# Kernel optimization log

Hardware: AMD Instinct MI355X
Metric: run time of the kernel (lower is better)

## Reference

```python
import jax, jax.numpy as jnp
import numpy as np

D_MODEL = 1024
N_HEADS = 16
N_KV_HEADS = 4
D_K = D_MODEL // N_HEADS
Q_SIZE = D_MODEL
KV_SIZE = N_KV_HEADS * D_K
QKV_SIZE = Q_SIZE + 2 * KV_SIZE
EPS = 1.1920929e-07  # torch.nn.RMSNorm default eps (fp32 machine eps)
ROPE_BASE = 10000.0


def rms_norm(x, w):
    # normalize over last dim, learned scale (torch nn.RMSNorm)
    return x * jax.lax.rsqrt(jnp.mean(x * x, axis=-1, keepdims=True) + EPS) * w


def rope(x):
    # torchtune RotaryPositionalEmbeddings: interleaved pairs, x is [B,T,H,D]
    T, d = x.shape[1], x.shape[-1]
    inv_freq = 1.0 / (ROPE_BASE ** (jnp.arange(0, d, 2, dtype=jnp.float32) / d))
    ang = jnp.arange(T, dtype=jnp.float32)[:, None] * inv_freq[None, :]  # [T, d/2]
    cos = jnp.cos(ang)[None, :, None, :]
    sin = jnp.sin(ang)[None, :, None, :]
    xr = x.reshape(x.shape[:-1] + (d // 2, 2))
    x1, x2 = xr[..., 0], xr[..., 1]
    out = jnp.stack([x1 * cos - x2 * sin, x1 * sin + x2 * cos], axis=-1)
    return out.reshape(x.shape)


def setup_inputs() -> dict:
    key = jax.random.key(0)
    k1, k2 = jax.random.split(key)
    x = jax.random.normal(k1, (2, 2048, D_MODEL), dtype=jnp.float32)
    qkvo = jax.random.normal(k2, (QKV_SIZE + D_MODEL, D_MODEL), dtype=jnp.float32) * 0.02
    q_norm_w = jnp.ones((D_K,), dtype=jnp.float32)
    k_norm_w = jnp.ones((D_K,), dtype=jnp.float32)
    return {"x": x, "qkvo": qkvo, "q_norm_w": q_norm_w, "k_norm_w": k_norm_w}


def reference(x, qkvo, q_norm_w, k_norm_w):
    B, T, _ = x.shape
    groups = N_HEADS // N_KV_HEADS
    qkv = x @ qkvo[:QKV_SIZE].T  # [B,T,qkv_size]
    Q = qkv[..., :Q_SIZE].reshape(B, T, N_HEADS, D_K)
    K = qkv[..., Q_SIZE:Q_SIZE + KV_SIZE].reshape(B, T, N_KV_HEADS, D_K)
    V = qkv[..., Q_SIZE + KV_SIZE:].reshape(B, T, N_KV_HEADS, D_K)
    Q = rope(rms_norm(Q, q_norm_w))
    K = rope(rms_norm(K, k_norm_w))
    K = jnp.repeat(K, groups, axis=2)  # GQA expand to [B,T,H,D]
    V = jnp.repeat(V, groups, axis=2)
    scale = 1.0 / np.sqrt(D_K).astype(np.float32)
    scores = jnp.einsum('bqhd,bkhd->bhqk', Q, K) * scale
    causal = jnp.tril(jnp.ones((T, T), dtype=bool))
    scores = jnp.where(causal[None, None], scores, jnp.float32(-jnp.inf))
    attn = jax.nn.softmax(scores, axis=-1)
    out = jnp.einsum('bhqk,bkhd->bqhd', attn, V).reshape(B, T, D_MODEL)
    return out @ qkvo[QKV_SIZE:].T
```

## Files before the change

kernel.cpp:

```cpp
#include <hip/hip_runtime.h>
#include <hip/hip_bf16.h>
#include <cstdint>
#include <cstddef>

typedef __bf16 bf16x8 __attribute__((ext_vector_type(8)));
typedef float f32x4 __attribute__((ext_vector_type(4)));

__device__ __forceinline__ unsigned short f2bf(float f) {
    unsigned u = __builtin_bit_cast(unsigned, f);
    u += 0x7FFFu + ((u >> 16) & 1u);
    return (unsigned short)(u >> 16);
}
__device__ __forceinline__ unsigned pk2(float a, float b) {
    typedef __bf16 bf16x2 __attribute__((ext_vector_type(2)));
    bf16x2 h;
    h[0] = (__bf16)a;
    h[1] = (__bf16)b;
    unsigned r;
    __builtin_memcpy(&r, &h, 4);
    return r;
}
__device__ __forceinline__ float fexp2(float x) {
#if __has_builtin(__builtin_amdgcn_exp2f)
    return __builtin_amdgcn_exp2f(x);
#else
    return __expf(x * 0.6931471805599453f);
#endif
}
__device__ __forceinline__ void gld16(const void* g, void* l) {
    __builtin_amdgcn_global_load_lds((const __attribute__((address_space(1))) void*)g,
                                     (__attribute__((address_space(3))) void*)l, 16, 0, 0);
}

__global__ __launch_bounds__(256) void cast_kernel(const float4* __restrict__ x,
                                                   const float4* __restrict__ w,
                                                   ushort4* __restrict__ xbf,
                                                   ushort4* __restrict__ wbf) {
    int i = blockIdx.x * 256 + threadIdx.x;
    const int NX4 = 4096 * 1024 / 4;
    const int NW4 = 2560 * 1024 / 4;
    float4 v;
    ushort4* o;
    if (i < NX4) { v = x[i]; o = xbf + i; }
    else {
        int j = i - NX4;
        if (j >= NW4) return;
        v = w[j]; o = wbf + j;
    }
    ushort4 r;
    r.x = f2bf(v.x); r.y = f2bf(v.y); r.z = f2bf(v.z); r.w = f2bf(v.w);
    *o = r;
}

__global__ __launch_bounds__(256) void gemm_bf16(const ushort* __restrict__ A,
                                                 const ushort* __restrict__ B,
                                                 float* __restrict__ C,
                                                 int M, int N, int K) {
    __shared__ __align__(16) ushort LA[2][4096];
    __shared__ __align__(16) ushort LB[2][8192];
    int tid = threadIdx.x;
    int w = tid >> 6, lane = tid & 63;
    int qm = lane & 15, quad = lane >> 4;

    int nbx = gridDim.x, nby = gridDim.y;
    int nwg = nbx * nby;
    int f = blockIdx.y * nbx + blockIdx.x;
    int q = nwg >> 3, r = nwg & 7;
    int xcd = f & 7, idx = f >> 3;
    int s = (xcd < r ? xcd * (q + 1) : r * (q + 1) + (xcd - r) * q) + idx;
    int m0 = (s / nby) * 64;
    int n0 = (s % nby) * 128;

    int mw = (w & 1) * 32, nw = (w >> 1) * 64;
    int sw = qm & 7;

    f32x4 acc[2][4];
#pragma unroll
    for (int i = 0; i < 2; i++)
#pragma unroll
        for (int j = 0; j < 4; j++) acc[i][j] = (f32x4){0.f, 0.f, 0.f, 0.f};

    int sa[2], ra[2], ga[2];
#pragma unroll
    for (int u = 0; u < 2; u++) {
        sa[u] = tid + u * 256;
        ra[u] = sa[u] >> 3;
        ga[u] = (sa[u] & 7) ^ (ra[u] & 7);
    }
    int sb[4], rb[4], gb[4];
#pragma unroll
    for (int u = 0; u < 4; u++) {
        sb[u] = tid + u * 256;
        rb[u] = sb[u] >> 3;
        gb[u] = (sb[u] & 7) ^ (rb[u] & 7);
    }

    auto do_stage = [&](int k0, int buf) {
#pragma unroll
        for (int u = 0; u < 2; u++)
            gld16(A + (size_t)(m0 + ra[u]) * K + k0 + ga[u] * 8, &LA[buf][sa[u] * 8]);
#pragma unroll
        for (int u = 0; u < 4; u++)
            gld16(B + (size_t)(n0 + rb[u]) * K + k0 + gb[u] * 8, &LB[buf][sb[u] * 8]);
    };

    do_stage(0, 0);
    int buf = 0;
    for (int k0 = 0; k0 < K; k0 += 64, buf ^= 1) {
        __syncthreads();
        if (k0 + 64 < K) do_stage(k0 + 64, buf ^ 1);
        bf16x8 a[2][2], bb[4][2];
#pragma unroll
        for (int mi = 0; mi < 2; mi++)
#pragma unroll
            for (int h = 0; h < 2; h++)
                a[mi][h] = *(const bf16x8*)&LA[buf][((mw + mi * 16 + qm) * 8 + ((h * 4 + quad) ^ sw)) * 8];
#pragma unroll
        for (int ni = 0; ni < 4; ni++)
#pragma unroll
            for (int h = 0; h < 2; h++)
                bb[ni][h] = *(const bf16x8*)&LB[buf][((nw + ni * 16 + qm) * 8 + ((h * 4 + quad) ^ sw)) * 8];
#pragma unroll
        for (int h = 0; h < 2; h++)
#pragma unroll
            for (int mi = 0; mi < 2; mi++)
#pragma unroll
                for (int ni = 0; ni < 4; ni++)
                    acc[mi][ni] = __builtin_amdgcn_mfma_f32_16x16x32_bf16(a[mi][h], bb[ni][h], acc[mi][ni], 0, 0, 0);
    }
#pragma unroll
    for (int mi = 0; mi < 2; mi++)
#pragma unroll
        for (int ni = 0; ni < 4; ni++) {
            int row = m0 + mw + mi * 16 + quad * 4;
            int col = n0 + nw + ni * 16 + qm;
            float* cp = C + (size_t)row * N + col;
#pragma unroll
            for (int r2 = 0; r2 < 4; r2++) cp[(size_t)r2 * N] = acc[mi][ni][r2];
        }
}

__global__ __launch_bounds__(256) void normrope_kernel(const float* __restrict__ qkv,
                                                       const float* __restrict__ qw,
                                                       const float* __restrict__ kw,
                                                       ushort* __restrict__ Q,
                                                       ushort* __restrict__ Kb) {
    int r = blockIdx.x;
    int b = r >> 11;
    int t = r & 2047;
    int tid = threadIdx.x;
    int w = tid >> 6;
    int lane = tid & 63;

    float inv_freq = __expf(-((float)(lane & 62) * (1.0f / 64.0f)) * 9.210340371976184f);
    float sn, cs;
    sincosf((float)t * inv_freq, &sn, &cs);

#pragma unroll
    for (int hg = 0; hg < 5; hg++) {
        int col = hg * 256 + w * 64 + lane;
        float v = qkv[(size_t)r * 1536 + col];
        float ss = v * v;
#pragma unroll
        for (int m = 1; m < 64; m <<= 1) ss += __shfl_xor(ss, m);
        float rinv = rsqrtf(ss * (1.0f / 64.0f) + 1.1920929e-7f);
        float wt = (hg < 4) ? qw[lane] : kw[lane];
        float vn = v * rinv * wt;
        float pr = __shfl_xor(vn, 1);
        float out = (lane & 1) ? fmaf(pr, sn, vn * cs) : fmaf(vn, cs, -pr * sn);
        if (hg < 4) {
            int h = hg * 4 + w;
            Q[((size_t)(b * 16 + h) * 2048 + t) * 64 + lane] = f2bf(out * 0.125f);
        } else {
            Kb[((size_t)(b * 4 + w) * 2048 + t) * 64 + lane] = f2bf(out);
        }
    }
}

__global__ __launch_bounds__(256) void vtrans_kernel(const float* __restrict__ qkv,
                                                     ushort* __restrict__ VT) {
    __shared__ float tile[64][65];
    int bkv = blockIdx.x;
    int t0 = blockIdx.y * 64;
    int b = bkv >> 2;
    int kvh = bkv & 3;
    int tid = threadIdx.x;
    int c = tid & 63;
    int rr = tid >> 6;
#pragma unroll
    for (int p = 0; p < 16; p++) {
        int tl = p * 4 + rr;
        tile[tl][c] = qkv[((size_t)(b * 2048) + t0 + tl) * 1536 + 1280 + kvh * 64 + c];
    }
    __syncthreads();
    int w5 = c & 31;
    int pc = (c & 32) + ((w5 >> 2) & 3) * 8 + (w5 >> 4) * 4 + (w5 & 3);
#pragma unroll
    for (int p = 0; p < 16; p++) {
        int dd = p * 4 + rr;
        VT[((size_t)bkv * 64 + dd) * 2048 + t0 + pc] = f2bf(tile[c][dd]);
    }
}

__global__ __launch_bounds__(256) void attn7_kernel(const ushort* __restrict__ Q,
                                                    const ushort* __restrict__ K,
                                                    const ushort* __restrict__ VT,
                                                    ushort* __restrict__ O) {
    __shared__ __align__(16) ushort KT[2][4096];
    __shared__ __align__(16) ushort VL[2][4096];

    const float LOG2E = 1.4426950408889634f;
    const float C8 = 11.541560327111707f;

    int blk = blockIdx.x;
    int qp = 31 - (blk >> 5);
    int bh = blk & 31;
    int tid = threadIdx.x;
    int w = tid >> 6, lane = tid & 63;
    int qm = lane & 15, quad = lane >> 4;
    int b = bh >> 4, h = bh & 15;
    int bkv = b * 4 + (h >> 2);

    const ushort* Qbh = Q + (size_t)bh * 2048 * 64;
    const ushort* Kbh = K + (size_t)bkv * 2048 * 64;
    const ushort* Vbh = VT + (size_t)bkv * 64 * 2048;
    int sw = qm & 7;

    int s0 = tid, s1 = tid + 256;
    int r0 = s0 >> 3, g0 = (s0 & 7) ^ (r0 & 7);
    int r1 = s1 >> 3, g1 = (s1 & 7) ^ (r1 & 7);

    auto do_stage = [&](int j0, int buf) {
        gld16(Kbh + (size_t)(j0 + r0) * 64 + g0 * 8, &KT[buf][s0 * 8]);
        gld16(Kbh + (size_t)(j0 + r1) * 64 + g1 * 8, &KT[buf][s1 * 8]);
        gld16(Vbh + (size_t)r0 * 2048 + j0 + g0 * 8, &VL[buf][s0 * 8]);
        gld16(Vbh + (size_t)r1 * 2048 + j0 + g1 * 8, &VL[buf][s1 * 8]);
    };

    int nch = qp + 1;
    int q0 = qp * 64 + w * 16;
    const ushort* qptr = Qbh + (size_t)(q0 + qm) * 64 + quad * 8;
    bf16x8 qb0 = *(const bf16x8*)qptr;
    bf16x8 qb1 = *(const bf16x8*)(qptr + 32);
    f32x4 oacc[4];
    float lacc = 0.f;
#pragma unroll
    for (int i = 0; i < 4; i++) oacc[i] = (f32x4){0.f, 0.f, 0.f, 0.f};

    do_stage(0, 0);
    int buf = 0;
#pragma unroll 1
    for (int i = 0; i < nch; i++, buf ^= 1) {
        int j0 = i * 64;
        __syncthreads();
        if (i + 1 < nch) do_stage(j0 + 64, buf ^ 1);

        f32x4 st[4];
#pragma unroll
        for (int tj = 0; tj < 4; tj++) st[tj] = (f32x4){0.f, 0.f, 0.f, 0.f};
#pragma unroll
        for (int tj = 0; tj < 4; tj++) {
            bf16x8 kf0 = *(const bf16x8*)&KT[buf][((16 * tj + qm) * 8 + (quad ^ sw)) * 8];
            bf16x8 kf1 = *(const bf16x8*)&KT[buf][((16 * tj + qm) * 8 + ((4 + quad) ^ sw)) * 8];
            st[tj] = __builtin_amdgcn_mfma_f32_16x16x32_bf16(kf0, qb0, st[tj], 0, 0, 0);
            st[tj] = __builtin_amdgcn_mfma_f32_16x16x32_bf16(kf1, qb1, st[tj], 0, 0, 0);
        }
        if (i == nch - 1) {
#pragma unroll
            for (int tj = 0; tj < 4; tj++)
#pragma unroll
                for (int r = 0; r < 4; r++) {
                    int key = j0 + tj * 16 + quad * 4 + r;
                    if (key > q0 + qm) st[tj][r] = -1e30f;
                }
        }
        float rs = 0.f;
#pragma unroll
        for (int tj = 0; tj < 4; tj++)
#pragma unroll
            for (int r = 0; r < 4; r++) {
                float pv = fexp2(fmaf(st[tj][r], LOG2E, -C8));
                st[tj][r] = pv;
                rs += pv;
            }
        lacc += rs;

        unsigned up[4];
        up[0] = pk2(st[0][0], st[0][1]);
        up[1] = pk2(st[0][2], st[0][3]);
        up[2] = pk2(st[1][0], st[1][1]);
        up[3] = pk2(st[1][2], st[1][3]);
        bf16x8 pf0;
        __builtin_memcpy(&pf0, up, 16);
        up[0] = pk2(st[2][0], st[2][1]);
        up[1] = pk2(st[2][2], st[2][3]);
        up[2] = pk2(st[3][0], st[3][1]);
        up[3] = pk2(st[3][2], st[3][3]);
        bf16x8 pf1;
        __builtin_memcpy(&pf1, up, 16);

#pragma unroll
        for (int dt = 0; dt < 4; dt++) {
            bf16x8 vf0 = *(const bf16x8*)&VL[buf][((16 * dt + qm) * 8 + (quad ^ sw)) * 8];
            bf16x8 vf1 = *(const bf16x8*)&VL[buf][((16 * dt + qm) * 8 + ((4 + quad) ^ sw)) * 8];
            oacc[dt] = __builtin_amdgcn_mfma_f32_16x16x32_bf16(vf0, pf0, oacc[dt], 0, 0, 0);
            oacc[dt] = __builtin_amdgcn_mfma_f32_16x16x32_bf16(vf1, pf1, oacc[dt], 0, 0, 0);
        }
    }
    float l = lacc;
    l += __shfl_xor(l, 16);
    l += __shfl_xor(l, 32);
    float rinv = 1.0f / l;
    uint2 val;
#pragma unroll
    for (int dt = 0; dt < 4; dt++) {
        val.x = pk2(oacc[dt][0] * rinv, oacc[dt][1] * rinv);
        val.y = pk2(oacc[dt][2] * rinv, oacc[dt][3] * rinv);
        *(uint2*)&O[((size_t)(b * 2048) + q0 + qm) * 1024 + h * 64 + dt * 16 + quad * 4] = val;
    }
}

extern "C" void kernel_launch(void* const* d_in, const int* in_sizes, int n_in,
                              void* d_out, int out_size, void* d_ws, size_t ws_size,
                              hipStream_t stream) {
    (void)in_sizes; (void)n_in; (void)out_size; (void)ws_size;
    const float* x    = (const float*)d_in[0];
    const float* qkvo = (const float*)d_in[1];
    const float* qw   = (const float*)d_in[2];
    const float* kw   = (const float*)d_in[3];
    float* out = (float*)d_out;

    char* ws = (char*)d_ws;
    ushort* xbf = (ushort*)(ws + 0);
    ushort* wbf = (ushort*)(ws + 8388608);
    float*  qkv = (float*)(ws + 13631488);
    ushort* Qb  = (ushort*)(ws + 38797312);
    ushort* Kb  = (ushort*)(ws + 47185920);
    ushort* VT  = (ushort*)(ws + 49283072);
    ushort* Ob  = (ushort*)(ws + 51380224);

    cast_kernel<<<6656, 256, 0, stream>>>((const float4*)x, (const float4*)qkvo,
                                          (ushort4*)xbf, (ushort4*)wbf);
    gemm_bf16<<<dim3(64, 12), 256, 0, stream>>>(xbf, wbf, qkv, 4096, 1536, 1024);
    normrope_kernel<<<4096, 256, 0, stream>>>(qkv, qw, kw, Qb, Kb);
    vtrans_kernel<<<dim3(8, 32), 256, 0, stream>>>(qkv, VT);
    attn7_kernel<<<1024, 256, 0, stream>>>(Qb, Kb, VT, Ob);
    gemm_bf16<<<dim3(64, 8), 256, 0, stream>>>(Ob, wbf + (size_t)1536 * 1024, out, 4096, 1024, 1024);
}
```

Before: 157.2 us.

## Fuse RMSNorm, RoPE and V transpose into the QKV GEMM epilogue

The QKV projection GEMM now applies per-head RMSNorm, RoPE and the Q scaling directly in registers, and writes bf16 Q/K in head-major layout. V tiles go through LDS and are written transposed and permuted for the attention kernel. This removes the fp32 qkv intermediate round trip and two separate kernel launches. The cast kernel also precomputes a cos/sin table for RoPE. In exchange the GEMM epilogue does more shuffles and scattered table reads and has a data-dependent branch per tile.

```diff
diff --git a/kernel.cpp b/kernel.cpp
--- a/kernel.cpp
+++ b/kernel.cpp
@@ -35,21 +35,175 @@
 __global__ __launch_bounds__(256) void cast_kernel(const float4* __restrict__ x,
                                                    const float4* __restrict__ w,
                                                    ushort4* __restrict__ xbf,
-                                                   ushort4* __restrict__ wbf) {
+                                                   ushort4* __restrict__ wbf,
+                                                   float2* __restrict__ tab) {
     int i = blockIdx.x * 256 + threadIdx.x;
     const int NX4 = 4096 * 1024 / 4;
     const int NW4 = 2560 * 1024 / 4;
-    float4 v;
-    ushort4* o;
-    if (i < NX4) { v = x[i]; o = xbf + i; }
-    else {
-        int j = i - NX4;
-        if (j >= NW4) return;
-        v = w[j]; o = wbf + j;
-    }
-    ushort4 r;
-    r.x = f2bf(v.x); r.y = f2bf(v.y); r.z = f2bf(v.z); r.w = f2bf(v.w);
-    *o = r;
+    if (i < NX4 + NW4) {
+        float4 v;
+        ushort4* o;
+        if (i < NX4) { v = x[i]; o = xbf + i; }
+        else { v = w[i - NX4]; o = wbf + (i - NX4); }
+        ushort4 r;
+        r.x = f2bf(v.x); r.y = f2bf(v.y); r.z = f2bf(v.z); r.w = f2bf(v.w);
+        *o = r;
+    } else {
+        int k = i - NX4 - NW4;
+        if (k >= 2048 * 32) return;
+        int t = k >> 5, fp = k & 31;
+        float inv = __expf(-(float)(2 * fp) * (1.0f / 64.0f) * 9.210340371976184f);
+        float sn, cs;
+        sincosf((float)t * inv, &sn, &cs);
+        tab[k] = make_float2(cs, sn);
+    }
+}
+
+__global__ __launch_bounds__(256) void gemm_qkv_fused(const ushort* __restrict__ A,
+                                                      const ushort* __restrict__ B,
+                                                      const float2* __restrict__ tab,
+                                                      const float* __restrict__ qw,
+                                                      const float* __restrict__ kw,
+                                                      ushort* __restrict__ Qo,
+                                                      ushort* __restrict__ Ko,
+                                                      ushort* __restrict__ VT) {
+    const int K = 1024;
+    __shared__ __align__(16) ushort LA[2][4096];
+    __shared__ __align__(16) ushort LB[2][8192];
+    int tid = threadIdx.x;
+    int w = tid >> 6, lane = tid & 63;
+    int qm = lane & 15, quad = lane >> 4;
+
+    int nbx = gridDim.x, nby = gridDim.y;
+    int nwg = nbx * nby;
+    int f = blockIdx.y * nbx + blockIdx.x;
+    int q = nwg >> 3, r = nwg & 7;
+    int xcd = f & 7, idx = f >> 3;
+    int s = (xcd < r ? xcd * (q + 1) : r * (q + 1) + (xcd - r) * q) + idx;
+    int m0 = (s / nby) * 64;
+    int n0 = (s % nby) * 128;
+
+    int mw = (w & 1) * 32, nw = (w >> 1) * 64;
+    int sw = qm & 7;
+
+    f32x4 acc[2][4];
+#pragma unroll
+    for (int i = 0; i < 2; i++)
+#pragma unroll
+        for (int j = 0; j < 4; j++) acc[i][j] = (f32x4){0.f, 0.f, 0.f, 0.f};
+
+    int sa[2], ra[2], ga[2];
+#pragma unroll
+    for (int u = 0; u < 2; u++) {
+        sa[u] = tid + u * 256;
+        ra[u] = sa[u] >> 3;
+        ga[u] = (sa[u] & 7) ^ (ra[u] & 7);
+    }
+    int sb[4], rb[4], gb[4];
+#pragma unroll
+    for (int u = 0; u < 4; u++) {
+        sb[u] = tid + u * 256;
+        rb[u] = sb[u] >> 3;
+        gb[u] = (sb[u] & 7) ^ (rb[u] & 7);
+    }
+
+    auto do_stage = [&](int k0, int buf) {
+#pragma unroll
+        for (int u = 0; u < 2; u++)
+            gld16(A + (size_t)(m0 + ra[u]) * K + k0 + ga[u] * 8, &LA[buf][sa[u] * 8]);
+#pragma unroll
+        for (int u = 0; u < 4; u++)
+            gld16(B + (size_t)(n0 + rb[u]) * K + k0 + gb[u] * 8, &LB[buf][sb[u] * 8]);
+    };
+
+    do_stage(0, 0);
+    int buf = 0;
+    for (int k0 = 0; k0 < K; k0 += 64, buf ^= 1) {
+        __syncthreads();
+        if (k0 + 64 < K) do_stage(k0 + 64, buf ^ 1);
+        bf16x8 a[2][2], bb[4][2];
+#pragma unroll
+        for (int mi = 0; mi < 2; mi++)
+#pragma unroll
+            for (int h = 0; h < 2; h++)
+                a[mi][h] = *(const bf16x8*)&LA[buf][((mw + mi * 16 + qm) * 8 + ((h * 4 + quad) ^ sw)) * 8];
+#pragma unroll
+        for (int ni = 0; ni < 4; ni++)
+#pragma unroll
+            for (int h = 0; h < 2; h++)
+                bb[ni][h] = *(const bf16x8*)&LB[buf][((nw + ni * 16 + qm) * 8 + ((h * 4 + quad) ^ sw)) * 8];
+#pragma unroll
+        for (int h = 0; h < 2; h++)
+#pragma unroll
+            for (int mi = 0; mi < 2; mi++)
+#pragma unroll
+                for (int ni = 0; ni < 4; ni++)
+                    acc[mi][ni] = __builtin_amdgcn_mfma_f32_16x16x32_bf16(a[mi][h], bb[ni][h], acc[mi][ni], 0, 0, 0);
+    }
+
+    int head_col0 = n0 + nw;
+    int rowbase = m0 + mw;
+    int b = rowbase >> 11;
+    int t0g = rowbase & 2047;
+    bool isV = (head_col0 >= 1280);
+
+    __syncthreads();
+    if (isV) {
+        ushort* lv = &LA[0][0] + w * 2048;
+#pragma unroll
+        for (int mi = 0; mi < 2; mi++)
+#pragma unroll
+            for (int r2 = 0; r2 < 4; r2++) {
+                int tt = mi * 16 + quad * 4 + r2;
+                int pcl = ((tt >> 2) & 3) * 8 + ((tt >> 4) & 1) * 4 + (tt & 3);
+#pragma unroll
+                for (int ni = 0; ni < 4; ni++)
+                    lv[(ni * 16 + qm) * 32 + pcl] = f2bf(acc[mi][ni][r2]);
+            }
+    } else {
+        bool isQ = (head_col0 < 1024);
+        const float* wp = isQ ? qw : kw;
+        float wt[4];
+#pragma unroll
+        for (int ni = 0; ni < 4; ni++) wt[ni] = wp[ni * 16 + qm];
+        float qs = isQ ? 0.125f : 1.0f;
+        ushort* op = isQ ? (Qo + (size_t)(b * 16 + (head_col0 >> 6)) * 2048 * 64)
+                         : (Ko + (size_t)(b * 4 + ((head_col0 - 1024) >> 6)) * 2048 * 64);
+#pragma unroll
+        for (int mi = 0; mi < 2; mi++)
+#pragma unroll
+            for (int r2 = 0; r2 < 4; r2++) {
+                float ssum = acc[mi][0][r2] * acc[mi][0][r2] + acc[mi][1][r2] * acc[mi][1][r2]
+                           + acc[mi][2][r2] * acc[mi][2][r2] + acc[mi][3][r2] * acc[mi][3][r2];
+                ssum += __shfl_xor(ssum, 1);
+                ssum += __shfl_xor(ssum, 2);
+                ssum += __shfl_xor(ssum, 4);
+                ssum += __shfl_xor(ssum, 8);
+                float rinv = rsqrtf(ssum * (1.0f / 64.0f) + 1.1920929e-7f);
+                int t = t0g + mi * 16 + quad * 4 + r2;
+#pragma unroll
+                for (int ni = 0; ni < 4; ni++) {
+                    float vn = acc[mi][ni][r2] * rinv * wt[ni];
+                    float2 cssn = tab[t * 32 + ni * 8 + (qm >> 1)];
+                    float pr = __shfl_xor(vn, 1);
+                    float out = (qm & 1) ? fmaf(pr, cssn.y, vn * cssn.x)
+                                         : fmaf(vn, cssn.x, -pr * cssn.y);
+                    op[(size_t)t * 64 + ni * 16 + qm] = f2bf(out * qs);
+                }
+            }
+    }
+    __syncthreads();
+    if (isV) {
+        const ushort* lv = &LA[0][0] + w * 2048;
+        int vh = (head_col0 - 1280) >> 6;
+        int bkv = b * 4 + vh;
+#pragma unroll
+        for (int j = 0; j < 8; j++) {
+            int d = j * 8 + (lane >> 3);
+            uint2 v = *(const uint2*)&lv[d * 32 + (lane & 7) * 4];
+            *(uint2*)&VT[((size_t)(bkv * 64 + d)) * 2048 + t0g + (lane & 7) * 4] = v;
+        }
+    }
 }
 
 __global__ __launch_bounds__(256) void gemm_bf16(const ushort* __restrict__ A,
@@ -138,68 +292,6 @@
 #pragma unroll
             for (int r2 = 0; r2 < 4; r2++) cp[(size_t)r2 * N] = acc[mi][ni][r2];
         }
-}
-
-__global__ __launch_bounds__(256) void normrope_kernel(const float* __restrict__ qkv,
-                                                       const float* __restrict__ qw,
-                                                       const float* __restrict__ kw,
-                                                       ushort* __restrict__ Q,
-                                                       ushort* __restrict__ Kb) {
-    int r = blockIdx.x;
-    int b = r >> 11;
-    int t = r & 2047;
-    int tid = threadIdx.x;
-    int w = tid >> 6;
-    int lane = tid & 63;
-
-    float inv_freq = __expf(-((float)(lane & 62) * (1.0f / 64.0f)) * 9.210340371976184f);
-    float sn, cs;
-    sincosf((float)t * inv_freq, &sn, &cs);
-
-#pragma unroll
-    for (int hg = 0; hg < 5; hg++) {
-        int col = hg * 256 + w * 64 + lane;
-        float v = qkv[(size_t)r * 1536 + col];
-        float ss = v * v;
-#pragma unroll
-        for (int m = 1; m < 64; m <<= 1) ss += __shfl_xor(ss, m);
-        float rinv = rsqrtf(ss * (1.0f / 64.0f) + 1.1920929e-7f);
-        float wt = (hg < 4) ? qw[lane] : kw[lane];
-        float vn = v * rinv * wt;
-        float pr = __shfl_xor(vn, 1);
-        float out = (lane & 1) ? fmaf(pr, sn, vn * cs) : fmaf(vn, cs, -pr * sn);
-        if (hg < 4) {
-            int h = hg * 4 + w;
-            Q[((size_t)(b * 16 + h) * 2048 + t) * 64 + lane] = f2bf(out * 0.125f);
-        } else {
-            Kb[((size_t)(b * 4 + w) * 2048 + t) * 64 + lane] = f2bf(out);
-        }
-    }
-}
-
-__global__ __launch_bounds__(256) void vtrans_kernel(const float* __restrict__ qkv,
-                                                     ushort* __restrict__ VT) {
-    __shared__ float tile[64][65];
-    int bkv = blockIdx.x;
-    int t0 = blockIdx.y * 64;
-    int b = bkv >> 2;
-    int kvh = bkv & 3;
-    int tid = threadIdx.x;
-    int c = tid & 63;
-    int rr = tid >> 6;
-#pragma unroll
-    for (int p = 0; p < 16; p++) {
-        int tl = p * 4 + rr;
-        tile[tl][c] = qkv[((size_t)(b * 2048) + t0 + tl) * 1536 + 1280 + kvh * 64 + c];
-    }
-    __syncthreads();
-    int w5 = c & 31;
-    int pc = (c & 32) + ((w5 >> 2) & 3) * 8 + (w5 >> 4) * 4 + (w5 & 3);
-#pragma unroll
-    for (int p = 0; p < 16; p++) {
-        int dd = p * 4 + rr;
-        VT[((size_t)bkv * 64 + dd) * 2048 + t0 + pc] = f2bf(tile[c][dd]);
-    }
 }
 
 __global__ __launch_bounds__(256) void attn7_kernel(const ushort* __restrict__ Q,
@@ -333,17 +425,15 @@
     char* ws = (char*)d_ws;
     ushort* xbf = (ushort*)(ws + 0);
     ushort* wbf = (ushort*)(ws + 8388608);
-    float*  qkv = (float*)(ws + 13631488);
+    float2* tab = (float2*)(ws + 13631488);
     ushort* Qb  = (ushort*)(ws + 38797312);
     ushort* Kb  = (ushort*)(ws + 47185920);
     ushort* VT  = (ushort*)(ws + 49283072);
     ushort* Ob  = (ushort*)(ws + 51380224);
 
-    cast_kernel<<<6656, 256, 0, stream>>>((const float4*)x, (const float4*)qkvo,
-                                          (ushort4*)xbf, (ushort4*)wbf);
-    gemm_bf16<<<dim3(64, 12), 256, 0, stream>>>(xbf, wbf, qkv, 4096, 1536, 1024);
-    normrope_kernel<<<4096, 256, 0, stream>>>(qkv, qw, kw, Qb, Kb);
-    vtrans_kernel<<<dim3(8, 32), 256, 0, stream>>>(qkv, VT);
+    cast_kernel<<<6912, 256, 0, stream>>>((const float4*)x, (const float4*)qkvo,
+                                          (ushort4*)xbf, (ushort4*)wbf, tab);
+    gemm_qkv_fused<<<dim3(64, 12), 256, 0, stream>>>(xbf, wbf, tab, qw, kw, Qb, Kb, VT);
     attn7_kernel<<<1024, 256, 0, stream>>>(Qb, Kb, VT, Ob);
     gemm_bf16<<<dim3(64, 8), 256, 0, stream>>>(Ob, wbf + (size_t)1536 * 1024, out, 4096, 1024, 1024);
 }
```

After: 152.5 us. 3.0% less time.
